# Performance work log

Hardware: AMD Instinct MI355X
Metric: run time of the kernel (lower is better)

Reference implementation:

```python
import jax, jax.numpy as jnp
import numpy as np

B = 1024
E = 200          # entity_dim (== relation_dim)
R = 200          # relation_dim
NE = 50000       # num_entities
NR = 400         # num_relations
OC = 32          # out_channels
FW = 9           # filt_w (filt_h = 1)
WP = E - FW + 1  # conv output width = 192
FC_IN = OC * WP  # 6144
EPS = 1e-5


def setup_inputs() -> dict:
    key = jax.random.key(0)
    ks = jax.random.split(key, 20)
    s = lambda n: 1.0 / np.sqrt(n)
    inp = {
        "e_s": jax.random.randint(ks[0], (B,), 0, NE, dtype=jnp.int32),
        "q_s": jax.random.randint(ks[1], (B,), 0, NR, dtype=jnp.int32),
        "e_c": jax.random.randint(ks[2], (B,), 0, NE, dtype=jnp.int32),
        "entity_emb": jax.random.normal(ks[3], (NE, E), jnp.float32) * 0.1,
        "relation_emb": jax.random.normal(ks[4], (NR, R), jnp.float32) * 0.1,
        "W1_w": jax.random.normal(ks[5], (E + R, R), jnp.float32) * s(E + R),
        "W1_b": jnp.zeros((R,), jnp.float32),
        "fc1_w": jax.random.normal(ks[6], (R, OC * FW), jnp.float32) * s(R),
        "fc1_b": jnp.zeros((OC * FW,), jnp.float32),
        "fc_w": jax.random.normal(ks[7], (FC_IN, E), jnp.float32) * s(FC_IN),
        "fc_b": jnp.zeros((E,), jnp.float32),
        "bn0_g": jnp.ones((1,), jnp.float32),
        "bn0_b": jnp.zeros((1,), jnp.float32),
        "bn0_m": jnp.zeros((1,), jnp.float32),
        "bn0_v": jnp.ones((1,), jnp.float32),
        "bn1_g": jnp.ones((OC,), jnp.float32),
        "bn1_b": jnp.zeros((OC,), jnp.float32),
        "bn1_m": jnp.zeros((OC,), jnp.float32),
        "bn1_v": jnp.ones((OC,), jnp.float32),
        "bn2_g": jnp.ones((E,), jnp.float32),
        "bn2_b": jnp.zeros((E,), jnp.float32),
        "bn2_m": jnp.zeros((E,), jnp.float32),
        "bn2_v": jnp.ones((E,), jnp.float32),
        "bias_b": jnp.zeros((NE,), jnp.float32),
    }
    return inp


def reference(e_s, q_s, e_c, entity_emb, relation_emb, W1_w, W1_b,
              fc1_w, fc1_b, fc_w, fc_b,
              bn0_g, bn0_b, bn0_m, bn0_v,
              bn1_g, bn1_b, bn1_m, bn1_v,
              bn2_g, bn2_b, bn2_m, bn2_v, bias_b):
    es = entity_emb[e_s]                      # [B,E]
    ec = entity_emb[e_c]                      # [B,E]
    r = relation_emb[q_s]                     # [B,R]
    # W1: Linear(E+R -> R); here R == E so e1 has width E
    e1 = jnp.concatenate([es, ec], -1) @ W1_w + W1_b          # [B,E]
    # bn0: single channel, inference mode
    x = (e1 - bn0_m) * (bn0_g / jnp.sqrt(bn0_v + EPS)) + bn0_b  # [B,E]
    # per-sample dynamic filters from fc1(r)
    k = (r @ fc1_w + fc1_b).reshape(B, OC, FW)                # [B,OC,FW]
    # grouped conv (groups=B) == per-sample 1D sliding dot products
    patches = jnp.stack([x[:, w:w + WP] for w in range(FW)], axis=-1)  # [B,WP,FW]
    conv = jnp.einsum('bpw,bow->bop', patches, k)             # [B,OC,WP]
    # bn1 over the OC channel, inference mode
    conv = (conv - bn1_m[:, None]) * (bn1_g / jnp.sqrt(bn1_v + EPS))[:, None] + bn1_b[:, None]
    flat = conv.reshape(B, FC_IN)                             # [B, OC*WP]
    h = flat @ fc_w + fc_b                                    # [B,E]
    h = (h - bn2_m) * (bn2_g / jnp.sqrt(bn2_v + EPS)) + bn2_b
    h = jax.nn.relu(h)
    logits = h @ entity_emb.T + bias_b                        # [B,NE]
    return jax.nn.sigmoid(logits)
```

## Files before the change

kernel.cpp:

```cpp
#include <hip/hip_runtime.h>

#define B_   1024
#define E_   200
#define NE_  50000
#define OC_  32
#define FW_  9
#define WP_  192
#define FCIN 6144
#define CATK 400
#define KDIM 288

typedef __attribute__((ext_vector_type(8))) short short8;
typedef __attribute__((ext_vector_type(4))) float floatx4;
typedef __attribute__((ext_vector_type(4))) unsigned short ushort4v;

static __device__ __forceinline__ float bf2f(unsigned short u) {
  return __uint_as_float(((unsigned)u) << 16);
}
static __device__ __forceinline__ unsigned short f2bf(float f) {
  unsigned u = __float_as_uint(f);
  u += 0x7FFFu + ((u >> 16) & 1u);
  return (unsigned short)(u >> 16);
}

#define PREP_GATH_BLKS  2400
#define PREP_W1_BLKS    28
#define PREP_FC1_BLKS   20
#define PREP_FCW_BLKS   384
#define PREP_R2 (PREP_GATH_BLKS)
#define PREP_R3 (PREP_R2 + PREP_W1_BLKS)
#define PREP_R4 (PREP_R3 + PREP_FC1_BLKS)
#define PREP_TOTAL (PREP_R4 + PREP_FCW_BLKS)

static __device__ __forceinline__ void transpose_region(
    const float* __restrict__ in, unsigned short* __restrict__ out,
    int N, int Npad, int K, int bx, int by,
    unsigned short (*lds)[65]) {
  int n0 = bx * 64, k0 = by * 64;
  int tx = threadIdx.x & 63, ty = threadIdx.x >> 6;
#pragma unroll
  for (int kk = 0; kk < 16; kk++) {
    int k = k0 + ty + 4 * kk;
    int n = n0 + tx;
    unsigned short v = 0;
    if (k < K && n < N) v = f2bf(in[(long)k * N + n]);
    lds[ty + 4 * kk][tx] = v;
  }
  __syncthreads();
#pragma unroll
  for (int kk = 0; kk < 16; kk++) {
    int k = k0 + tx;
    int n = n0 + ty + 4 * kk;
    if (n < Npad && k < K) out[(long)n * K + k] = lds[tx][ty + 4 * kk];
  }
}

__global__ __launch_bounds__(256) void k_prep(
    const float* __restrict__ ent, const float* __restrict__ rel,
    const int* __restrict__ e_s, const int* __restrict__ q_s, const int* __restrict__ e_c,
    const float* __restrict__ W1w, const float* __restrict__ fc1w, const float* __restrict__ fcw,
    unsigned short* __restrict__ cat, unsigned short* __restrict__ rbuf,
    unsigned short* __restrict__ W1T, unsigned short* __restrict__ fc1T,
    unsigned short* __restrict__ fcwT) {
  __shared__ unsigned short lds[64][65];
  int blk = blockIdx.x, tid = threadIdx.x;
  if (blk < PREP_R2) {
    int idx = blk * 256 + tid;
    if (idx < B_ * CATK) {
      int s = idx / CATK, i = idx - s * CATK;
      int row = (i < E_) ? e_s[s] : e_c[s];
      int col = (i < E_) ? i : i - E_;
      cat[idx] = f2bf(ent[row * E_ + col]);
    } else {
      int j = idx - B_ * CATK;
      int s = j / E_, i = j - s * E_;
      rbuf[j] = f2bf(rel[q_s[s] * E_ + i]);
    }
  } else if (blk < PREP_R3) {
    int l = blk - PREP_R2;
    transpose_region(W1w, W1T, 200, 208, CATK, l % 4, l / 4, lds);
  } else if (blk < PREP_R4) {
    int l = blk - PREP_R3;
    transpose_region(fc1w, fc1T, 288, 288, E_, l % 5, l / 5, lds);
  } else {
    int l = blk - PREP_R4;
    transpose_region(fcw, fcwT, 200, 208, FCIN, l % 4, l / 4, lds);
  }
}

template<int NK, int RQ>
static __device__ __forceinline__ floatx4 gemm_64x16(
    const unsigned short* __restrict__ A, int lda,
    const unsigned short* __restrict__ Bt, int ldb, int m0, int n0) {
  int lane = threadIdx.x & 63;
  int wv   = threadIdx.x >> 6;
  int l16  = lane & 15, quad = lane >> 4;
  const unsigned short* ap = A  + (long)(m0 + 16 * wv + l16) * lda + quad * 8;
  const unsigned short* bp = Bt + (long)(n0 + l16) * ldb + quad * 8;
  floatx4 acc = {0.f, 0.f, 0.f, 0.f};
#pragma unroll 4
  for (int ks = 0; ks < NK; ks++) {
    short8 a = *(const short8*)(ap + ks * 32);
    short8 b = *(const short8*)(bp + ks * 32);
    acc = __builtin_amdgcn_mfma_f32_16x16x32_bf16(a, b, acc, 0, 0, 0);
  }
  if (RQ > 0) {
    short8 z = {0,0,0,0,0,0,0,0};
    short8 a = (quad < RQ) ? *(const short8*)(ap + NK * 32) : z;
    short8 b = (quad < RQ) ? *(const short8*)(bp + NK * 32) : z;
    acc = __builtin_amdgcn_mfma_f32_16x16x32_bf16(a, b, acc, 0, 0, 0);
  }
  return acc;
}

__global__ __launch_bounds__(256) void k_gemm_ek(
    const unsigned short* __restrict__ cat, const unsigned short* __restrict__ W1T,
    const float* __restrict__ W1b,
    const float* __restrict__ g0, const float* __restrict__ b0,
    const float* __restrict__ m0p, const float* __restrict__ v0,
    unsigned short* __restrict__ xbuf,
    const unsigned short* __restrict__ rbuf, const unsigned short* __restrict__ fc1T,
    const float* __restrict__ fc1b,
    const float* __restrict__ g1, const float* __restrict__ v1,
    unsigned short* __restrict__ kbuf) {
  int blk = blockIdx.x;
  int lane = threadIdx.x & 63, wv = threadIdx.x >> 6;
  int l16 = lane & 15, quad = lane >> 4;
  if (blk < 208) {
    int m0 = (blk & 15) * 64, n0 = (blk >> 4) * 16;
    floatx4 acc = gemm_64x16<12, 2>(cat, CATK, W1T, CATK, m0, n0);
    int j = n0 + l16;
    if (j < E_) {
      float s0  = g0[0] * rsqrtf(v0[0] + 1e-5f);
      float off = (W1b[j] - m0p[0]) * s0 + b0[0];
      int rbase = m0 + 16 * wv + quad * 4;
#pragma unroll
      for (int i = 0; i < 4; i++)
        xbuf[(rbase + i) * E_ + j] = f2bf(acc[i] * s0 + off);
    }
  } else {
    int l = blk - 208;
    int m0 = (l & 15) * 64, n0 = (l >> 4) * 16;
    floatx4 acc = gemm_64x16<6, 1>(rbuf, E_, fc1T, E_, m0, n0);
    int c = n0 + l16;
    int o = c / FW_;
    float s1 = g1[o] * rsqrtf(v1[o] + 1e-5f);
    float fb = fc1b[c];
    int rbase = m0 + 16 * wv + quad * 4;
#pragma unroll
    for (int i = 0; i < 4; i++)
      kbuf[(rbase + i) * KDIM + c] = f2bf((acc[i] + fb) * s1);
  }
}

#define CVT_BLKS 9766
__global__ __launch_bounds__(256) void k_conv(
    const unsigned short* __restrict__ xbuf, const unsigned short* __restrict__ kbuf,
    const float* __restrict__ g1, const float* __restrict__ b1,
    const float* __restrict__ m1, const float* __restrict__ v1,
    unsigned short* __restrict__ flat,
    const float* __restrict__ ent, unsigned short* __restrict__ entb) {
  __shared__ float xs[E_];
  __shared__ float ks[KDIM];
  __shared__ float beta[OC_];
  int tid = threadIdx.x;
  if (blockIdx.x >= B_) {
    int i = (blockIdx.x - B_) * 256 + tid;
    if (i < NE_ * E_ / 4) {
      float4 v = ((const float4*)ent)[i];
      ushort4v o = {f2bf(v.x), f2bf(v.y), f2bf(v.z), f2bf(v.w)};
      __builtin_nontemporal_store(o, (ushort4v*)entb + i);
    }
    return;
  }
  int b = blockIdx.x;
  if (tid < E_)  xs[tid] = bf2f(xbuf[b * E_ + tid]);
  for (int i = tid; i < KDIM; i += 256) ks[i] = bf2f(kbuf[b * KDIM + i]);
  if (tid < OC_) {
    float s = g1[tid] * rsqrtf(v1[tid] + 1e-5f);
    beta[tid] = b1[tid] - m1[tid] * s;
  }
  __syncthreads();
  int o = tid >> 3, pc = tid & 7;
  int p0 = pc * 24;
  float kw[FW_];
#pragma unroll
  for (int w = 0; w < FW_; w++) kw[w] = ks[o * FW_ + w];
  float xw[32];
#pragma unroll
  for (int q = 0; q < 8; q++) {
    float4 v = *(const float4*)&xs[p0 + 4 * q];
    xw[4 * q + 0] = v.x; xw[4 * q + 1] = v.y; xw[4 * q + 2] = v.z; xw[4 * q + 3] = v.w;
  }
  float bo = beta[o];
  unsigned short* fp = flat + b * FCIN + o * WP_ + p0;
#pragma unroll
  for (int j = 0; j < 24; j += 2) {
    float a0 = bo, a1 = bo;
#pragma unroll
    for (int w = 0; w < FW_; w++) {
      a0 += xw[j + w] * kw[w];
      a1 += xw[j + 1 + w] * kw[w];
    }
    unsigned pack = (unsigned)f2bf(a0) | ((unsigned)f2bf(a1) << 16);
    *(unsigned*)(fp + j) = pack;
  }
}

__global__ __launch_bounds__(512) void k_gemm_fc2(
    const unsigned short* __restrict__ flat, const unsigned short* __restrict__ fcwT,
    const float* __restrict__ fcb,
    const float* __restrict__ g2, const float* __restrict__ b2,
    const float* __restrict__ m2, const float* __restrict__ v2,
    unsigned short* __restrict__ hbuf) {
  __shared__ float red[8][32][17];
  int m0 = blockIdx.x * 32, n0 = blockIdx.y * 16;
  int tid = threadIdx.x;
  int lane = tid & 63, kc = tid >> 6;
  int l16 = lane & 15, quad = lane >> 4;
  const unsigned short* ap0 = flat + (long)(m0 + l16) * FCIN + kc * 768 + quad * 8;
  const unsigned short* ap1 = ap0 + 16 * FCIN;
  const unsigned short* bp  = fcwT + (long)(n0 + l16) * FCIN + kc * 768 + quad * 8;
  floatx4 acc0 = {0.f, 0.f, 0.f, 0.f};
  floatx4 acc1 = {0.f, 0.f, 0.f, 0.f};
#pragma unroll 4
  for (int ks = 0; ks < 24; ks++) {
    short8 b  = *(const short8*)(bp  + ks * 32);
    short8 a0 = *(const short8*)(ap0 + ks * 32);
    short8 a1 = *(const short8*)(ap1 + ks * 32);
    acc0 = __builtin_amdgcn_mfma_f32_16x16x32_bf16(a0, b, acc0, 0, 0, 0);
    acc1 = __builtin_amdgcn_mfma_f32_16x16x32_bf16(a1, b, acc1, 0, 0, 0);
  }
#pragma unroll
  for (int i = 0; i < 4; i++) {
    red[kc][quad * 4 + i][l16]      = acc0[i];
    red[kc][16 + quad * 4 + i][l16] = acc1[i];
  }
  __syncthreads();
  int row = tid >> 4, col = tid & 15;
  float s = 0.f;
#pragma unroll
  for (int k2 = 0; k2 < 8; k2++) s += red[k2][row][col];
  int j = n0 + col;
  if (j < E_) {
    float s2 = g2[j] * rsqrtf(v2[j] + 1e-5f);
    float h = (s + fcb[j] - m2[j]) * s2 + b2[j];
    hbuf[(m0 + row) * E_ + j] = f2bf(fmaxf(h, 0.f));
  }
}

__global__ __launch_bounds__(512, 4) void k_gemm_out(
    const unsigned short* __restrict__ hbuf, const unsigned short* __restrict__ entb,
    const float* __restrict__ bias, float* __restrict__ out) {
  __shared__ __align__(16) unsigned short Blds[7 * 4 * 128 * 8];
  int g = blockIdx.x;
  int xcd = g & 7, local_ = g >> 3;
  int T = (xcd < 4 ? xcd * 196 : 784 + (xcd - 4) * 195) + local_;
  int mt = T & 3, nt = T >> 2;
  int m0 = mt * 256, n0 = nt * 128;
  int tid = threadIdx.x;

#pragma unroll
  for (int it = 0; it < 7; ++it) {
    int idx = it * 512 + tid;
    int ks = idx >> 9, qd = (idx >> 7) & 3, np = idx & 127;
    int col = 8 * (np & 15) + (np >> 4);
    int n = n0 + col;
    int kb = ks * 32 + qd * 8;
    short8 v = {0, 0, 0, 0, 0, 0, 0, 0};
    if (kb < 200 && n < NE_) v = *(const short8*)(entb + (long)n * E_ + kb);
    *(short8*)(Blds + idx * 8) = v;
  }
  __syncthreads();

  int lane = tid & 63, wv = tid >> 6;
  int l16 = lane & 15, quad = lane >> 4;
  const unsigned short* ap0 = hbuf + (long)(m0 + wv * 32 + l16) * E_ + quad * 8;
  const unsigned short* ap1 = ap0 + 16 * E_;

  floatx4 acc[16];
#pragma unroll
  for (int i = 0; i < 16; ++i) acc[i] = (floatx4){0.f, 0.f, 0.f, 0.f};

#pragma unroll
  for (int ks = 0; ks < 6; ++ks) {
    short8 a0 = *(const short8*)(ap0 + ks * 32);
    short8 a1 = *(const short8*)(ap1 + ks * 32);
    const unsigned short* bb = Blds + (ks * 4 + quad) * 1024 + l16 * 8;
#pragma unroll
    for (int nf = 0; nf < 8; ++nf) {
      short8 b = *(const short8*)(bb + nf * 128);
      acc[nf]     = __builtin_amdgcn_mfma_f32_16x16x32_bf16(a0, b, acc[nf], 0, 0, 0);
      acc[8 + nf] = __builtin_amdgcn_mfma_f32_16x16x32_bf16(a1, b, acc[8 + nf], 0, 0, 0);
    }
  }
  {
    short8 z = {0, 0, 0, 0, 0, 0, 0, 0};
    short8 a0 = (quad == 0) ? *(const short8*)(ap0 + 192) : z;
    short8 a1 = (quad == 0) ? *(const short8*)(ap1 + 192) : z;
    const unsigned short* bb = Blds + (24 + quad) * 1024 + l16 * 8;
#pragma unroll
    for (int nf = 0; nf < 8; ++nf) {
      short8 b = *(const short8*)(bb + nf * 128);
      acc[nf]     = __builtin_amdgcn_mfma_f32_16x16x32_bf16(a0, b, acc[nf], 0, 0, 0);
      acc[8 + nf] = __builtin_amdgcn_mfma_f32_16x16x32_bf16(a1, b, acc[8 + nf], 0, 0, 0);
    }
  }

  int nb = n0 + 8 * l16;
  if (nb >= NE_) return;
  float4 bi0 = *(const float4*)(bias + nb);
  float4 bi1 = *(const float4*)(bias + nb + 4);
#pragma unroll
  for (int mf = 0; mf < 2; ++mf) {
#pragma unroll
    for (int i = 0; i < 4; ++i) {
      int row = m0 + wv * 32 + mf * 16 + quad * 4 + i;
      floatx4 v0, v1;
      v0.x = 1.f / (1.f + __expf(-(acc[mf * 8 + 0][i] + bi0.x)));
      v0.y = 1.f / (1.f + __expf(-(acc[mf * 8 + 1][i] + bi0.y)));
      v0.z = 1.f / (1.f + __expf(-(acc[mf * 8 + 2][i] + bi0.z)));
      v0.w = 1.f / (1.f + __expf(-(acc[mf * 8 + 3][i] + bi0.w)));
      v1.x = 1.f / (1.f + __expf(-(acc[mf * 8 + 4][i] + bi1.x)));
      v1.y = 1.f / (1.f + __expf(-(acc[mf * 8 + 5][i] + bi1.y)));
      v1.z = 1.f / (1.f + __expf(-(acc[mf * 8 + 6][i] + bi1.z)));
      v1.w = 1.f / (1.f + __expf(-(acc[mf * 8 + 7][i] + bi1.w)));
      float* op = out + (long)row * NE_ + nb;
      __builtin_nontemporal_store(v0, (floatx4*)op);
      __builtin_nontemporal_store(v1, (floatx4*)(op + 4));
    }
  }
}

extern "C" void kernel_launch(void* const* d_in, const int* in_sizes, int n_in,
                              void* d_out, int out_size, void* d_ws, size_t ws_size,
                              hipStream_t stream) {
  const int* e_s = (const int*)d_in[0];
  const int* q_s = (const int*)d_in[1];
  const int* e_c = (const int*)d_in[2];
  const float* ent  = (const float*)d_in[3];
  const float* rel  = (const float*)d_in[4];
  const float* W1w  = (const float*)d_in[5];
  const float* W1b  = (const float*)d_in[6];
  const float* fc1w = (const float*)d_in[7];
  const float* fc1b = (const float*)d_in[8];
  const float* fcw  = (const float*)d_in[9];
  const float* fcb  = (const float*)d_in[10];
  const float* g0 = (const float*)d_in[11];
  const float* b0 = (const float*)d_in[12];
  const float* m0 = (const float*)d_in[13];
  const float* v0 = (const float*)d_in[14];
  const float* g1 = (const float*)d_in[15];
  const float* b1 = (const float*)d_in[16];
  const float* m1 = (const float*)d_in[17];
  const float* v1 = (const float*)d_in[18];
  const float* g2 = (const float*)d_in[19];
  const float* b2 = (const float*)d_in[20];
  const float* m2 = (const float*)d_in[21];
  const float* v2 = (const float*)d_in[22];
  const float* bias = (const float*)d_in[23];
  float* out = (float*)d_out;

  char* w = (char*)d_ws;
  unsigned short* entb = (unsigned short*)(w + 0);
  unsigned short* cat  = (unsigned short*)(w + 20000256);
  unsigned short* rbuf = (unsigned short*)(w + 20819712);
  unsigned short* W1T  = (unsigned short*)(w + 21229568);
  unsigned short* fc1T = (unsigned short*)(w + 21396224);
  unsigned short* fcwT = (unsigned short*)(w + 21511680);
  unsigned short* xbuf = (unsigned short*)(w + 24067840);
  unsigned short* kbuf = (unsigned short*)(w + 24477696);
  unsigned short* flat = (unsigned short*)(w + 25067776);
  unsigned short* hbuf = (unsigned short*)(w + 37650944);

  k_prep<<<dim3(PREP_TOTAL), dim3(256), 0, stream>>>(
      ent, rel, e_s, q_s, e_c, W1w, fc1w, fcw, cat, rbuf, W1T, fc1T, fcwT);
  k_gemm_ek<<<dim3(496), dim3(256), 0, stream>>>(
      cat, W1T, W1b, g0, b0, m0, v0, xbuf, rbuf, fc1T, fc1b, g1, v1, kbuf);
  k_conv<<<dim3(B_ + CVT_BLKS), dim3(256), 0, stream>>>(
      xbuf, kbuf, g1, b1, m1, v1, flat, ent, entb);
  k_gemm_fc2<<<dim3(32, 13), dim3(512), 0, stream>>>(
      flat, fcwT, fcb, g2, b2, m2, v2, hbuf);
  k_gemm_out<<<dim3(1564), dim3(512), 0, stream>>>(hbuf, entb, bias, out);
}
```

Baseline: 400.6 us.

## Shrink output GEMM LDS tile, remap columns, and raise occupancy bound

The B tile in the output GEMM now stores only the 25 real K-chunks of the entity embedding instead of padding to 28, which cuts LDS per block. The launch-bounds occupancy hint rises from 4 to 6 blocks. Columns are remapped so each lane writes two float4 groups 64 columns apart rather than eight adjacent columns, and the edge guard is now per store. The intent is more resident blocks to hide the memory-bound sigmoid output writes, at the cost of fewer registers per thread and a possible change in store coalescing.

```diff
diff --git a/kernel.cpp b/kernel.cpp
--- a/kernel.cpp
+++ b/kernel.cpp
@@ -249,10 +249,10 @@
   }
 }
 
-__global__ __launch_bounds__(512, 4) void k_gemm_out(
+__global__ __launch_bounds__(512, 6) void k_gemm_out(
     const unsigned short* __restrict__ hbuf, const unsigned short* __restrict__ entb,
     const float* __restrict__ bias, float* __restrict__ out) {
-  __shared__ __align__(16) unsigned short Blds[7 * 4 * 128 * 8];
+  __shared__ __align__(16) unsigned short Blds[25 * 128 * 8];
   int g = blockIdx.x;
   int xcd = g & 7, local_ = g >> 3;
   int T = (xcd < 4 ? xcd * 196 : 784 + (xcd - 4) * 195) + local_;
@@ -263,13 +263,15 @@
 #pragma unroll
   for (int it = 0; it < 7; ++it) {
     int idx = it * 512 + tid;
-    int ks = idx >> 9, qd = (idx >> 7) & 3, np = idx & 127;
-    int col = 8 * (np & 15) + (np >> 4);
-    int n = n0 + col;
-    int kb = ks * 32 + qd * 8;
-    short8 v = {0, 0, 0, 0, 0, 0, 0, 0};
-    if (kb < 200 && n < NE_) v = *(const short8*)(entb + (long)n * E_ + kb);
-    *(short8*)(Blds + idx * 8) = v;
+    if (idx < 25 * 128) {
+      int c = idx >> 7, np = idx & 127;
+      int col = 4 * (np & 15) + ((np >> 4) & 3) + 64 * (np >> 6);
+      int n = n0 + col;
+      int kb = c * 8;
+      short8 v = {0, 0, 0, 0, 0, 0, 0, 0};
+      if (n < NE_) v = *(const short8*)(entb + (long)n * E_ + kb);
+      *(short8*)(Blds + idx * 8) = v;
+    }
   }
   __syncthreads();
 
@@ -298,19 +300,20 @@
     short8 z = {0, 0, 0, 0, 0, 0, 0, 0};
     short8 a0 = (quad == 0) ? *(const short8*)(ap0 + 192) : z;
     short8 a1 = (quad == 0) ? *(const short8*)(ap1 + 192) : z;
-    const unsigned short* bb = Blds + (24 + quad) * 1024 + l16 * 8;
+    const unsigned short* bbr = Blds + 24 * 1024 + l16 * 8;
 #pragma unroll
     for (int nf = 0; nf < 8; ++nf) {
-      short8 b = *(const short8*)(bb + nf * 128);
+      short8 b = (quad == 0) ? *(const short8*)(bbr + nf * 128) : z;
       acc[nf]     = __builtin_amdgcn_mfma_f32_16x16x32_bf16(a0, b, acc[nf], 0, 0, 0);
       acc[8 + nf] = __builtin_amdgcn_mfma_f32_16x16x32_bf16(a1, b, acc[8 + nf], 0, 0, 0);
     }
   }
 
-  int nb = n0 + 8 * l16;
-  if (nb >= NE_) return;
-  float4 bi0 = *(const float4*)(bias + nb);
-  float4 bi1 = *(const float4*)(bias + nb + 4);
+  int nb0 = n0 + 4 * l16;
+  int nb1 = nb0 + 64;
+  bool ok0 = nb0 < NE_, ok1 = nb1 < NE_;
+  float4 bi0 = ok0 ? *(const float4*)(bias + nb0) : make_float4(0.f, 0.f, 0.f, 0.f);
+  float4 bi1 = ok1 ? *(const float4*)(bias + nb1) : make_float4(0.f, 0.f, 0.f, 0.f);
 #pragma unroll
   for (int mf = 0; mf < 2; ++mf) {
 #pragma unroll
@@ -325,9 +328,9 @@
       v1.y = 1.f / (1.f + __expf(-(acc[mf * 8 + 5][i] + bi1.y)));
       v1.z = 1.f / (1.f + __expf(-(acc[mf * 8 + 6][i] + bi1.z)));
       v1.w = 1.f / (1.f + __expf(-(acc[mf * 8 + 7][i] + bi1.w)));
-      float* op = out + (long)row * NE_ + nb;
-      __builtin_nontemporal_store(v0, (floatx4*)op);
-      __builtin_nontemporal_store(v1, (floatx4*)(op + 4));
+      float* op = out + (long)row * NE_;
+      if (ok0) __builtin_nontemporal_store(v0, (floatx4*)(op + nb0));
+      if (ok1) __builtin_nontemporal_store(v1, (floatx4*)(op + nb1));
     }
   }
 }
```

Measured after the change: 485.0 us. 1.21x slower.
